# Kernel tuning notes

Measured on AMD Instinct MI355X. Metric: run time of the kernel, lower is better.

## Reference

```python
import jax, jax.numpy as jnp
import numpy as np

D_MODEL = 1024
NUM_HEADS = 16
D_K = D_MODEL // NUM_HEADS
B, S = 4, 2048


def setup_inputs() -> dict:
    key = jax.random.key(0)
    ks = jax.random.split(key, 9)
    scale = 1.0 / np.sqrt(D_MODEL)
    x = jax.random.normal(ks[0], (B, S, D_MODEL), dtype=jnp.float32)
    Wq = jax.random.uniform(ks[1], (D_MODEL, D_MODEL), jnp.float32, -scale, scale)
    bq = jax.random.uniform(ks[2], (D_MODEL,), jnp.float32, -scale, scale)
    Wk = jax.random.uniform(ks[3], (D_MODEL, D_MODEL), jnp.float32, -scale, scale)
    bk = jax.random.uniform(ks[4], (D_MODEL,), jnp.float32, -scale, scale)
    Wv = jax.random.uniform(ks[5], (D_MODEL, D_MODEL), jnp.float32, -scale, scale)
    bv = jax.random.uniform(ks[6], (D_MODEL,), jnp.float32, -scale, scale)
    Wo = jax.random.uniform(ks[7], (D_MODEL, D_MODEL), jnp.float32, -scale, scale)
    bo = jax.random.uniform(ks[8], (D_MODEL,), jnp.float32, -scale, scale)
    return {"x": x, "Wq": Wq, "bq": bq, "Wk": Wk, "bk": bk,
            "Wv": Wv, "bv": bv, "Wo": Wo, "bo": bo}


def reference(x, Wq, bq, Wk, bk, Wv, bv, Wo, bo):
    Bsz, Sl, _ = x.shape
    # Linear: x @ W.T + b (torch nn.Linear convention), then split heads -> (B,H,S,d_k)
    def proj(W, b):
        h = jnp.einsum('bsd,ed->bse', x, W) + b
        return h.reshape(Bsz, Sl, NUM_HEADS, D_K).transpose(0, 2, 1, 3)
    q = proj(Wq, bq)
    k = proj(Wk, bk)
    v = proj(Wv, bv)
    scores = jnp.einsum('bhqd,bhkd->bhqk', q, k) / np.sqrt(D_K)
    causal = jnp.tril(jnp.ones((Sl, Sl), dtype=bool))  # True = keep
    scores = jnp.where(causal[None, None], scores, -jnp.inf)
    attn = jax.nn.softmax(scores, axis=-1)
    out = jnp.einsum('bhqk,bhkd->bhqd', attn, v)
    out = out.transpose(0, 2, 1, 3).reshape(Bsz, Sl, D_MODEL)
    return jnp.einsum('bsd,ed->bse', out, Wo) + bo
```

## Files before the change

### kernel.cpp

```cpp
#include <hip/hip_runtime.h>
#include <hip/hip_bf16.h>

typedef __attribute__((ext_vector_type(8))) short short8;
typedef __attribute__((ext_vector_type(4))) short short4v;
typedef __attribute__((ext_vector_type(4))) float floatx4;
typedef __attribute__((ext_vector_type(2))) unsigned int uint2v;
typedef unsigned short u16;

#define B_SZ 4
#define NH   16
#define SEQ  2048
#define DM   1024
#define DK   64
#define M_ROWS (B_SZ * SEQ)

__device__ __forceinline__ u16 f2bf(float f) {
  unsigned u = __float_as_uint(f);
  u += 0x7fff + ((u >> 16) & 1);
  return (u16)(u >> 16);
}

__device__ __forceinline__ unsigned cvt_pk_bf16(float lo, float hi) {
  unsigned r;
  asm("v_cvt_pk_bf16_f32 %0, %1, %2" : "=v"(r) : "v"(lo), "v"(hi));
  return r;
}

__device__ __forceinline__ void async_copy16(const u16* g, const short* lds) {
  __builtin_amdgcn_global_load_lds(
      (const __attribute__((address_space(1))) void*)g,
      (__attribute__((address_space(3))) void*)lds,
      16, 0, 0);
}

#define BAR() do { __builtin_amdgcn_s_barrier(); asm volatile("" ::: "memory"); } while (0)

__global__ __launch_bounds__(256)
void cvt4_kernel(const float* __restrict__ x,
                 const float* __restrict__ wq, const float* __restrict__ wk,
                 const float* __restrict__ wv,
                 u16* __restrict__ xb, u16* __restrict__ wb)
{
  const int y = blockIdx.y;
  const float* src; u16* dst; int n4;
  if (y == 0)      { src = x;  dst = xb;                 n4 = (M_ROWS * DM) / 4; }
  else if (y == 1) { src = wq; dst = wb;                 n4 = (DM * DM) / 4; }
  else if (y == 2) { src = wk; dst = wb + DM * DM;       n4 = (DM * DM) / 4; }
  else             { src = wv; dst = wb + 2 * DM * DM;   n4 = (DM * DM) / 4; }
  for (int i = blockIdx.x * 256 + threadIdx.x; i < n4; i += gridDim.x * 256) {
    floatx4 v = ((const floatx4*)src)[i];
    short4v s;
#pragma unroll
    for (int e = 0; e < 4; ++e) s[e] = (short)f2bf(v[e]);
    ((short4v*)dst)[i] = s;
  }
}

__global__ __launch_bounds__(256)
void cvt1_kernel(const float* __restrict__ in, u16* __restrict__ out, int n4)
{
  for (int i = blockIdx.x * 256 + threadIdx.x; i < n4; i += gridDim.x * 256) {
    floatx4 v = ((const floatx4*)in)[i];
    short4v s;
#pragma unroll
    for (int e = 0; e < 4; ++e) s[e] = (short)f2bf(v[e]);
    ((short4v*)out)[i] = s;
  }
}

__device__ __forceinline__ void stage_half32(
    const u16* __restrict__ src,
    short* dst,
    int wid, int lane)
{
  const int row = wid * 16 + (lane >> 2);
  const int cu  = (lane & 3) ^ ((lane >> 2) & 3) ^ ((lane >> 4) & 3);
  async_copy16(src + (size_t)row * DM + cu * 8, dst + wid * 512);
}

template<int MIF>
__device__ __forceinline__ void gemm256_core(
    const u16* __restrict__ A, const u16* __restrict__ B,
    int m0, int n0, floatx4 (&acc)[MIF][4])
{
  constexpr int ASH = MIF * 32 * 32;
  constexpr int AH  = MIF / 4;
  constexpr int L   = AH + 2;

  __shared__ short smem[2 * (ASH + 8192)];

  const int tid  = threadIdx.x;
  const int wid  = tid >> 6;
  const int lane = tid & 63;
  const int wm   = wid >> 2, wn = wid & 3;
  const int quad = lane >> 4, l16 = lane & 15;
  const int rswz = (l16 & 3) ^ ((l16 >> 2) & 3);

  short* sA_[2] = { smem,       smem + ASH + 8192 };
  short* sB_[2] = { smem + ASH, smem + 2 * ASH + 8192 };

#pragma unroll
  for (int mi = 0; mi < MIF; ++mi)
#pragma unroll
    for (int ni = 0; ni < 4; ++ni)
      acc[mi][ni] = floatx4{0.f, 0.f, 0.f, 0.f};

  const u16* Abase = A + (size_t)m0 * DM;
  const u16* Bbase = B + (size_t)n0 * DM;

#define STAGE_TILE(kof, c) do {                                              \
    _Pragma("unroll")                                                        \
    for (int u = 0; u < AH; ++u)                                             \
      stage_half32(Abase + (size_t)(u * 128) * DM + (kof),                   \
                   sA_[c] + u * 4096, wid, lane);                            \
    stage_half32(Bbase + (kof),                    sB_[c],        wid, lane); \
    stage_half32(Bbase + (size_t)128 * DM + (kof), sB_[c] + 4096, wid, lane); \
  } while (0)

#define VMCNT_L() do {                                                       \
    if constexpr (L == 4) asm volatile("s_waitcnt vmcnt(4)" ::: "memory");   \
    else                  asm volatile("s_waitcnt vmcnt(3)" ::: "memory");   \
  } while (0)

  STAGE_TILE(0, 0);
  STAGE_TILE(32, 1);
  VMCNT_L();
  BAR();

  short8 af[MIF], bf[4];

  for (int i = 0; i < 16; ++i) {
    const bool nl = (i < 15);
#pragma unroll
    for (int half = 0; half < 2; ++half) {
      short* cA = sA_[half];
      short* cB = sB_[half];
      const int kof_n = (2 * i + 2 + half) * 32;

#pragma unroll
      for (int nt = 0; nt < 2; ++nt)
        bf[nt] = *(const short8*)(cB + (wn * 64 + nt * 16 + l16) * 32
                                     + (((quad) ^ rswz) << 3));
#pragma unroll
      for (int mi = 0; mi < MIF / 2; ++mi)
        af[mi] = *(const short8*)(cA + (wm * (MIF * 16) + mi * 16 + l16) * 32
                                     + (((quad) ^ rswz) << 3));
#pragma unroll
      for (int nt = 2; nt < 4; ++nt)
        bf[nt] = *(const short8*)(cB + (wn * 64 + nt * 16 + l16) * 32
                                     + (((quad) ^ rswz) << 3));
#pragma unroll
      for (int mi = MIF / 2; mi < MIF; ++mi)
        af[mi] = *(const short8*)(cA + (wm * (MIF * 16) + mi * 16 + l16) * 32
                                     + (((quad) ^ rswz) << 3));

      __builtin_amdgcn_s_setprio(1);
#pragma unroll
      for (int mi = 0; mi < MIF / 2; ++mi)
#pragma unroll
        for (int nt = 0; nt < 2; ++nt)
          acc[mi][nt] = __builtin_amdgcn_mfma_f32_16x16x32_bf16(
              af[mi], bf[nt], acc[mi][nt], 0, 0, 0);
#pragma unroll
      for (int mi = 0; mi < MIF / 2; ++mi)
#pragma unroll
        for (int nt = 2; nt < 4; ++nt)
          acc[mi][nt] = __builtin_amdgcn_mfma_f32_16x16x32_bf16(
              af[mi], bf[nt], acc[mi][nt], 0, 0, 0);
#pragma unroll
      for (int mi = MIF / 2; mi < MIF; ++mi)
#pragma unroll
        for (int nt = 2; nt < 4; ++nt)
          acc[mi][nt] = __builtin_amdgcn_mfma_f32_16x16x32_bf16(
              af[mi], bf[nt], acc[mi][nt], 0, 0, 0);
      __builtin_amdgcn_s_setprio(0);

      BAR();

      if (nl) {
        STAGE_TILE(kof_n, half);
        VMCNT_L();
      } else {
        asm volatile("s_waitcnt vmcnt(0)" ::: "memory");
      }

      __builtin_amdgcn_s_setprio(1);
#pragma unroll
      for (int mi = MIF / 2; mi < MIF; ++mi)
#pragma unroll
        for (int nt = 0; nt < 2; ++nt)
          acc[mi][nt] = __builtin_amdgcn_mfma_f32_16x16x32_bf16(
              af[mi], bf[nt], acc[mi][nt], 0, 0, 0);
      __builtin_amdgcn_s_setprio(0);

      BAR();
    }
  }
#undef STAGE_TILE
#undef VMCNT_L
}

__global__ __launch_bounds__(512, 2)
void qkv256_kernel(const u16* __restrict__ xb, const u16* __restrict__ wb,
                   const float* __restrict__ bq, const float* __restrict__ bk,
                   const float* __restrict__ bv,
                   u16* __restrict__ Qo, u16* __restrict__ Ko, u16* __restrict__ Vto)
{
  const int bx = blockIdx.x;
  const int wg = (bx & 7) * 48 + (bx >> 3);
  const int mat = wg >> 7;
  const int r   = wg & 127;

  int m0, n0;
  const u16 *A, *Bm;
  if (mat < 2) { m0 = (r >> 2) * 256; n0 = (r & 3) * 256; A = xb; Bm = wb + (size_t)mat * DM * DM; }
  else         { m0 = (r & 3) * 256;  n0 = (r >> 2) * 256; A = wb + (size_t)2 * DM * DM; Bm = xb; }

  floatx4 acc[8][4];
  gemm256_core<8>(A, Bm, m0, n0, acc);

  const int tid = threadIdx.x;
  const int wid = tid >> 6, lane = tid & 63;
  const int wm = wid >> 2, wn = wid & 3;
  const int quad = lane >> 4, l16 = lane & 15;

  if (mat < 2) {
    u16* dst = (mat == 0) ? Qo : Ko;
    const float* bias = (mat == 0) ? bq : bk;
#pragma unroll
    for (int ni = 0; ni < 4; ++ni) {
      const int n = n0 + wn * 64 + ni * 16 + l16;
      const float bb = bias[n];
      const int h = n >> 6, d = n & 63;
#pragma unroll
      for (int mi = 0; mi < 8; ++mi)
#pragma unroll
        for (int rr = 0; rr < 4; ++rr) {
          const int m = m0 + wm * 128 + mi * 16 + quad * 4 + rr;
          const int b = m >> 11, s = m & 2047;
          dst[((size_t)(b * NH + h) * SEQ + s) * DK + d] = f2bf(acc[mi][ni][rr] + bb);
        }
    }
  } else {
#pragma unroll
    for (int mi = 0; mi < 8; ++mi)
#pragma unroll
      for (int rr = 0; rr < 4; ++rr) {
        const int m = m0 + wm * 128 + mi * 16 + quad * 4 + rr;
        const float bb = bv[m];
        const int h = m >> 6, d = m & 63;
#pragma unroll
        for (int ni = 0; ni < 4; ++ni) {
          const int n = n0 + wn * 64 + ni * 16 + l16;
          const int b = n >> 11, s = n & 2047;
          Vto[((size_t)(b * NH + h) * DK + d) * SEQ + s] = f2bf(acc[mi][ni][rr] + bb);
        }
      }
  }
}

#define AT_STR 72
__global__ __launch_bounds__(256, 2)
void attn_kernel(const u16* __restrict__ Q, const u16* __restrict__ Kx,
                 const u16* __restrict__ Vt, u16* __restrict__ O)
{
  __shared__ short Ks[64 * 64];
  __shared__ short Vs[64 * 64];
  __shared__ __align__(16) short Ps[4 * 16 * AT_STR];

  const int bh  = blockIdx.x;
  const int qtb = 15 - (int)blockIdx.y;
  const int q0  = qtb * 128;
  const int tid = threadIdx.x;
  const int w = tid >> 6, lane = tid & 63;
  const int quad = lane >> 4, l16 = lane & 15;
  const int r8 = lane >> 3, c8 = lane & 7;

  const u16* Qh = Q  + (size_t)bh * SEQ * DK;
  const u16* Kh = Kx + (size_t)bh * SEQ * DK;
  const u16* Vh = Vt + (size_t)bh * DK * SEQ;

  short8 qf[2][2];
#pragma unroll
  for (int qp = 0; qp < 2; ++qp) {
    const int qrow = q0 + w * 32 + qp * 16 + l16;
#pragma unroll
    for (int h = 0; h < 2; ++h)
      qf[qp][h] = *(const short8*)(Qh + (size_t)qrow * DK + h * 32 + quad * 8);
  }

  short8 vone;
#pragma unroll
  for (int j = 0; j < 8; ++j) vone[j] = (l16 == 0) ? (short)0x3F80 : (short)0;

  floatx4 o[2][4], ls[2];
#pragma unroll
  for (int qp = 0; qp < 2; ++qp) {
    ls[qp] = floatx4{0.f, 0.f, 0.f, 0.f};
#pragma unroll
    for (int dt = 0; dt < 4; ++dt) o[qp][dt] = floatx4{0.f, 0.f, 0.f, 0.f};
  }

  const float SC2 = 0.18033688011f;
  const int ktmax = 2 * qtb + 2;
  short* Pw = Ps + w * 16 * AT_STR;

  for (int kt = 0; kt < ktmax; ++kt) {
    const int k0 = kt * 64;
    __syncthreads();
#pragma unroll
    for (int c = 0; c < 2; ++c) {
      const int row8 = w * 16 + c * 8;
      const int sw   = (c8 ^ r8) * 8;
      async_copy16(Kh + (size_t)(k0 + row8 + r8) * DK + sw, Ks + row8 * 64);
      async_copy16(Vh + (size_t)(row8 + r8) * SEQ + k0 + sw, Vs + row8 * 64);
    }
    __syncthreads();

    short8 kf[4][2], vf[4][2];
#pragma unroll
    for (int nt = 0; nt < 4; ++nt)
#pragma unroll
      for (int h = 0; h < 2; ++h) {
        kf[nt][h] = *(const short8*)(Ks + (nt * 16 + l16) * 64 + (((h * 4 + quad) ^ (l16 & 7)) * 8));
        vf[nt][h] = *(const short8*)(Vs + (nt * 16 + l16) * 64 + (((h * 4 + quad) ^ (l16 & 7)) * 8));
      }

#pragma unroll
    for (int qp = 0; qp < 2; ++qp) {
      const int frag0 = q0 + w * 32 + qp * 16;
      if (k0 <= frag0 + 15) {
        floatx4 sc[4];
#pragma unroll
        for (int nt = 0; nt < 4; ++nt) {
          floatx4 z = floatx4{0.f, 0.f, 0.f, 0.f};
          z = __builtin_amdgcn_mfma_f32_16x16x32_bf16(kf[nt][0], qf[qp][0], z, 0, 0, 0);
          z = __builtin_amdgcn_mfma_f32_16x16x32_bf16(kf[nt][1], qf[qp][1], z, 0, 0, 0);
          sc[nt] = z;
        }
        const bool diag = (k0 + 63 > frag0);
        const int qrow = frag0 + l16;
#pragma unroll
        for (int nt = 0; nt < 4; ++nt)
#pragma unroll
          for (int r = 0; r < 4; ++r) {
            float s = sc[nt][r] * SC2;
            if (diag) {
              const int col = k0 + nt * 16 + quad * 4 + r;
              if (col > qrow) s = -1e30f;
            }
            sc[nt][r] = __builtin_amdgcn_exp2f(s);
          }
#pragma unroll
        for (int nt = 0; nt < 4; ++nt) {
          uint2v wv2;
          wv2[0] = cvt_pk_bf16(sc[nt][0], sc[nt][1]);
          wv2[1] = cvt_pk_bf16(sc[nt][2], sc[nt][3]);
          *(short4v*)(Pw + l16 * AT_STR + nt * 16 + quad * 4) =
              __builtin_bit_cast(short4v, wv2);
        }
        asm volatile("" ::: "memory");
        short8 pf[2];
#pragma unroll
        for (int h = 0; h < 2; ++h)
          pf[h] = *(const short8*)(Pw + l16 * AT_STR + h * 32 + quad * 8);
#pragma unroll
        for (int dt = 0; dt < 4; ++dt) {
          o[qp][dt] = __builtin_amdgcn_mfma_f32_16x16x32_bf16(pf[0], vf[dt][0], o[qp][dt], 0, 0, 0);
          o[qp][dt] = __builtin_amdgcn_mfma_f32_16x16x32_bf16(pf[1], vf[dt][1], o[qp][dt], 0, 0, 0);
        }
        ls[qp] = __builtin_amdgcn_mfma_f32_16x16x32_bf16(pf[0], vone, ls[qp], 0, 0, 0);
        ls[qp] = __builtin_amdgcn_mfma_f32_16x16x32_bf16(pf[1], vone, ls[qp], 0, 0, 0);
      }
    }
  }

  const int b = bh >> 4, h = bh & 15;
#pragma unroll
  for (int qp = 0; qp < 2; ++qp) {
    const int frag0 = q0 + w * 32 + qp * 16;
#pragma unroll
    for (int r = 0; r < 4; ++r) {
      const float lv  = __shfl(ls[qp][r], lane & 48);
      const float inv = 1.0f / fmaxf(lv, 1e-20f);
      const int row   = frag0 + quad * 4 + r;
      const size_t base = ((size_t)b * SEQ + row) * DM + h * DK;
#pragma unroll
      for (int dt = 0; dt < 4; ++dt)
        O[base + dt * 16 + l16] = f2bf(o[qp][dt][r] * inv);
    }
  }
}

__global__ __launch_bounds__(512, 2)
void oproj256_kernel(const u16* __restrict__ A, const u16* __restrict__ Wob,
                     const float* __restrict__ bo, float* __restrict__ out)
{
  const int bx = blockIdx.x;
  const int wg = (bx & 7) * 32 + (bx >> 3);
  const int m0 = (wg >> 2) * 128, n0 = (wg & 3) * 256;

  floatx4 acc[4][4];
  gemm256_core<4>(A, Wob, m0, n0, acc);

  const int tid = threadIdx.x;
  const int wid = tid >> 6, lane = tid & 63;
  const int wm = wid >> 2, wn = wid & 3;
  const int quad = lane >> 4, l16 = lane & 15;

#pragma unroll
  for (int ni = 0; ni < 4; ++ni) {
    const int n = n0 + wn * 64 + ni * 16 + l16;
    const float bb = bo[n];
#pragma unroll
    for (int mi = 0; mi < 4; ++mi)
#pragma unroll
      for (int rr = 0; rr < 4; ++rr) {
        const int m = m0 + wm * 64 + mi * 16 + quad * 4 + rr;
        out[(size_t)m * DM + n] = acc[mi][ni][rr] + bb;
      }
  }
}

extern "C" void kernel_launch(void* const* d_in, const int* in_sizes, int n_in,
                              void* d_out, int out_size, void* d_ws, size_t ws_size,
                              hipStream_t stream)
{
  const float* x  = (const float*)d_in[0];
  const float* Wq = (const float*)d_in[1];
  const float* bq = (const float*)d_in[2];
  const float* Wk = (const float*)d_in[3];
  const float* bk = (const float*)d_in[4];
  const float* Wv = (const float*)d_in[5];
  const float* bv = (const float*)d_in[6];
  const float* Wo = (const float*)d_in[7];
  const float* bo = (const float*)d_in[8];
  float* out = (float*)d_out;

  u16* qws  = (u16*)d_ws;
  u16* kws  = qws  + (size_t)M_ROWS * DM;
  u16* vtws = kws  + (size_t)M_ROWS * DM;
  u16* ows  = vtws + (size_t)M_ROWS * DM;

  u16* xb = (u16*)d_out;
  u16* wb = xb + (size_t)M_ROWS * DM;
  u16* wo_b = qws;

  cvt4_kernel  <<<dim3(1024, 4), 256, 0, stream>>>(x, Wq, Wk, Wv, xb, wb);
  qkv256_kernel<<<dim3(384), 512, 0, stream>>>(xb, wb, bq, bk, bv, qws, kws, vtws);
  attn_kernel  <<<dim3(64, 16), 256, 0, stream>>>(qws, kws, vtws, ows);
  cvt1_kernel  <<<dim3(1024), 256, 0, stream>>>(Wo, wo_b, (DM * DM) / 4);
  oproj256_kernel<<<dim3(256), 512, 0, stream>>>(ows, wo_b, bo, out);
}
```

Before: 259.9 us.

## Shrink QKV and output-projection GEMM tiles to 128x128 with 4-wave blocks

Replaces the 256-wide, 8-wave GEMM core with a 128x128 tile core using 4 waves, each computing 64x64. The QKV and output projections now launch four and two times as many blocks, respectively. The aim is better occupancy and finer load balance across CUs, with more blocks resident per CU. The trade is lower data reuse per tile, so more global and L2 traffic for the same FLOPs.

Measured after the change: 250.7 us. 3.5% less time.

```diff
diff --git a/kernel.cpp b/kernel.cpp
--- a/kernel.cpp
+++ b/kernel.cpp
@@ -68,39 +68,44 @@
   }
 }
 
-__device__ __forceinline__ void stage_half32(
-    const u16* __restrict__ src,
-    short* dst,
-    int wid, int lane)
-{
-  const int row = wid * 16 + (lane >> 2);
+__device__ __forceinline__ void stage_tile128(
+    const u16* __restrict__ Asrc, const u16* __restrict__ Bsrc,
+    short* sA, short* sB, int w, int lane)
+{
   const int cu  = (lane & 3) ^ ((lane >> 2) & 3) ^ ((lane >> 4) & 3);
-  async_copy16(src + (size_t)row * DM + cu * 8, dst + wid * 512);
-}
-
-template<int MIF>
-__device__ __forceinline__ void gemm256_core(
+  const int rlo = lane >> 2;
+#pragma unroll
+  for (int j = 0; j < 2; ++j) {
+    const int oct = w * 2 + j;
+    const int row = oct * 16 + rlo;
+    async_copy16(Asrc + (size_t)row * DM + cu * 8, sA + oct * 512);
+  }
+#pragma unroll
+  for (int j = 0; j < 2; ++j) {
+    const int oct = w * 2 + j;
+    const int row = oct * 16 + rlo;
+    async_copy16(Bsrc + (size_t)row * DM + cu * 8, sB + oct * 512);
+  }
+}
+
+__device__ __forceinline__ void gemm128_core(
     const u16* __restrict__ A, const u16* __restrict__ B,
-    int m0, int n0, floatx4 (&acc)[MIF][4])
-{
-  constexpr int ASH = MIF * 32 * 32;
-  constexpr int AH  = MIF / 4;
-  constexpr int L   = AH + 2;
-
-  __shared__ short smem[2 * (ASH + 8192)];
+    int m0, int n0, floatx4 (&acc)[4][4])
+{
+  __shared__ short smem[16384];
 
   const int tid  = threadIdx.x;
-  const int wid  = tid >> 6;
+  const int w    = tid >> 6;
   const int lane = tid & 63;
-  const int wm   = wid >> 2, wn = wid & 3;
+  const int wm   = w >> 1, wn = w & 1;
   const int quad = lane >> 4, l16 = lane & 15;
   const int rswz = (l16 & 3) ^ ((l16 >> 2) & 3);
 
-  short* sA_[2] = { smem,       smem + ASH + 8192 };
-  short* sB_[2] = { smem + ASH, smem + 2 * ASH + 8192 };
-
-#pragma unroll
-  for (int mi = 0; mi < MIF; ++mi)
+  short* sA_[2] = { smem,        smem + 8192 };
+  short* sB_[2] = { smem + 4096, smem + 12288 };
+
+#pragma unroll
+  for (int mi = 0; mi < 4; ++mi)
 #pragma unroll
     for (int ni = 0; ni < 4; ++ni)
       acc[mi][ni] = floatx4{0.f, 0.f, 0.f, 0.f};
@@ -108,26 +113,12 @@
   const u16* Abase = A + (size_t)m0 * DM;
   const u16* Bbase = B + (size_t)n0 * DM;
 
-#define STAGE_TILE(kof, c) do {                                              \
-    _Pragma("unroll")                                                        \
-    for (int u = 0; u < AH; ++u)                                             \
-      stage_half32(Abase + (size_t)(u * 128) * DM + (kof),                   \
-                   sA_[c] + u * 4096, wid, lane);                            \
-    stage_half32(Bbase + (kof),                    sB_[c],        wid, lane); \
-    stage_half32(Bbase + (size_t)128 * DM + (kof), sB_[c] + 4096, wid, lane); \
-  } while (0)
-
-#define VMCNT_L() do {                                                       \
-    if constexpr (L == 4) asm volatile("s_waitcnt vmcnt(4)" ::: "memory");   \
-    else                  asm volatile("s_waitcnt vmcnt(3)" ::: "memory");   \
-  } while (0)
-
-  STAGE_TILE(0, 0);
-  STAGE_TILE(32, 1);
-  VMCNT_L();
+  stage_tile128(Abase,      Bbase,      sA_[0], sB_[0], w, lane);
+  stage_tile128(Abase + 32, Bbase + 32, sA_[1], sB_[1], w, lane);
+  asm volatile("s_waitcnt vmcnt(4)" ::: "memory");
   BAR();
 
-  short8 af[MIF], bf[4];
+  short8 af[4], bf[4];
 
   for (int i = 0; i < 16; ++i) {
     const bool nl = (i < 15);
@@ -140,35 +131,25 @@
 #pragma unroll
       for (int nt = 0; nt < 2; ++nt)
         bf[nt] = *(const short8*)(cB + (wn * 64 + nt * 16 + l16) * 32
-                                     + (((quad) ^ rswz) << 3));
-#pragma unroll
-      for (int mi = 0; mi < MIF / 2; ++mi)
-        af[mi] = *(const short8*)(cA + (wm * (MIF * 16) + mi * 16 + l16) * 32
-                                     + (((quad) ^ rswz) << 3));
+                                     + ((quad ^ rswz) << 3));
+#pragma unroll
+      for (int mi = 0; mi < 4; ++mi)
+        af[mi] = *(const short8*)(cA + (wm * 64 + mi * 16 + l16) * 32
+                                     + ((quad ^ rswz) << 3));
 #pragma unroll
       for (int nt = 2; nt < 4; ++nt)
         bf[nt] = *(const short8*)(cB + (wn * 64 + nt * 16 + l16) * 32
-                                     + (((quad) ^ rswz) << 3));
-#pragma unroll
-      for (int mi = MIF / 2; mi < MIF; ++mi)
-        af[mi] = *(const short8*)(cA + (wm * (MIF * 16) + mi * 16 + l16) * 32
-                                     + (((quad) ^ rswz) << 3));
+                                     + ((quad ^ rswz) << 3));
 
       __builtin_amdgcn_s_setprio(1);
 #pragma unroll
-      for (int mi = 0; mi < MIF / 2; ++mi)
-#pragma unroll
-        for (int nt = 0; nt < 2; ++nt)
+      for (int mi = 0; mi < 2; ++mi)
+#pragma unroll
+        for (int nt = 0; nt < 4; ++nt)
           acc[mi][nt] = __builtin_amdgcn_mfma_f32_16x16x32_bf16(
               af[mi], bf[nt], acc[mi][nt], 0, 0, 0);
 #pragma unroll
-      for (int mi = 0; mi < MIF / 2; ++mi)
-#pragma unroll
-        for (int nt = 2; nt < 4; ++nt)
-          acc[mi][nt] = __builtin_amdgcn_mfma_f32_16x16x32_bf16(
-              af[mi], bf[nt], acc[mi][nt], 0, 0, 0);
-#pragma unroll
-      for (int mi = MIF / 2; mi < MIF; ++mi)
+      for (int mi = 2; mi < 4; ++mi)
 #pragma unroll
         for (int nt = 2; nt < 4; ++nt)
           acc[mi][nt] = __builtin_amdgcn_mfma_f32_16x16x32_bf16(
@@ -178,15 +159,15 @@
       BAR();
 
       if (nl) {
-        STAGE_TILE(kof_n, half);
-        VMCNT_L();
+        stage_tile128(Abase + kof_n, Bbase + kof_n, cA, cB, w, lane);
+        asm volatile("s_waitcnt vmcnt(4)" ::: "memory");
       } else {
         asm volatile("s_waitcnt vmcnt(0)" ::: "memory");
       }
 
       __builtin_amdgcn_s_setprio(1);
 #pragma unroll
-      for (int mi = MIF / 2; mi < MIF; ++mi)
+      for (int mi = 2; mi < 4; ++mi)
 #pragma unroll
         for (int nt = 0; nt < 2; ++nt)
           acc[mi][nt] = __builtin_amdgcn_mfma_f32_16x16x32_bf16(
@@ -196,32 +177,30 @@
       BAR();
     }
   }
-#undef STAGE_TILE
-#undef VMCNT_L
-}
-
-__global__ __launch_bounds__(512, 2)
-void qkv256_kernel(const u16* __restrict__ xb, const u16* __restrict__ wb,
+}
+
+__global__ __launch_bounds__(256, 4)
+void qkv128_kernel(const u16* __restrict__ xb, const u16* __restrict__ wb,
                    const float* __restrict__ bq, const float* __restrict__ bk,
                    const float* __restrict__ bv,
                    u16* __restrict__ Qo, u16* __restrict__ Ko, u16* __restrict__ Vto)
 {
   const int bx = blockIdx.x;
-  const int wg = (bx & 7) * 48 + (bx >> 3);
-  const int mat = wg >> 7;
-  const int r   = wg & 127;
+  const int wg = (bx & 7) * 192 + (bx >> 3);
+  const int mat = wg >> 9;
+  const int r   = wg & 511;
 
   int m0, n0;
   const u16 *A, *Bm;
-  if (mat < 2) { m0 = (r >> 2) * 256; n0 = (r & 3) * 256; A = xb; Bm = wb + (size_t)mat * DM * DM; }
-  else         { m0 = (r & 3) * 256;  n0 = (r >> 2) * 256; A = wb + (size_t)2 * DM * DM; Bm = xb; }
-
-  floatx4 acc[8][4];
-  gemm256_core<8>(A, Bm, m0, n0, acc);
+  if (mat < 2) { m0 = (r >> 3) * 128; n0 = (r & 7) * 128; A = xb; Bm = wb + (size_t)mat * DM * DM; }
+  else         { m0 = (r & 7) * 128;  n0 = (r >> 3) * 128; A = wb + (size_t)2 * DM * DM; Bm = xb; }
+
+  floatx4 acc[4][4];
+  gemm128_core(A, Bm, m0, n0, acc);
 
   const int tid = threadIdx.x;
-  const int wid = tid >> 6, lane = tid & 63;
-  const int wm = wid >> 2, wn = wid & 3;
+  const int w = tid >> 6, lane = tid & 63;
+  const int wm = w >> 1, wn = w & 1;
   const int quad = lane >> 4, l16 = lane & 15;
 
   if (mat < 2) {
@@ -233,20 +212,20 @@
       const float bb = bias[n];
       const int h = n >> 6, d = n & 63;
 #pragma unroll
-      for (int mi = 0; mi < 8; ++mi)
+      for (int mi = 0; mi < 4; ++mi)
 #pragma unroll
         for (int rr = 0; rr < 4; ++rr) {
-          const int m = m0 + wm * 128 + mi * 16 + quad * 4 + rr;
+          const int m = m0 + wm * 64 + mi * 16 + quad * 4 + rr;
           const int b = m >> 11, s = m & 2047;
           dst[((size_t)(b * NH + h) * SEQ + s) * DK + d] = f2bf(acc[mi][ni][rr] + bb);
         }
     }
   } else {
 #pragma unroll
-    for (int mi = 0; mi < 8; ++mi)
+    for (int mi = 0; mi < 4; ++mi)
 #pragma unroll
       for (int rr = 0; rr < 4; ++rr) {
-        const int m = m0 + wm * 128 + mi * 16 + quad * 4 + rr;
+        const int m = m0 + wm * 64 + mi * 16 + quad * 4 + rr;
         const float bb = bv[m];
         const int h = m >> 6, d = m & 63;
 #pragma unroll
@@ -392,20 +371,20 @@
   }
 }
 
-__global__ __launch_bounds__(512, 2)
-void oproj256_kernel(const u16* __restrict__ A, const u16* __restrict__ Wob,
+__global__ __launch_bounds__(256, 4)
+void oproj128_kernel(const u16* __restrict__ A, const u16* __restrict__ Wob,
                      const float* __restrict__ bo, float* __restrict__ out)
 {
   const int bx = blockIdx.x;
-  const int wg = (bx & 7) * 32 + (bx >> 3);
-  const int m0 = (wg >> 2) * 128, n0 = (wg & 3) * 256;
+  const int wg = (bx & 7) * 64 + (bx >> 3);
+  const int m0 = (wg >> 3) * 128, n0 = (wg & 7) * 128;
 
   floatx4 acc[4][4];
-  gemm256_core<4>(A, Wob, m0, n0, acc);
+  gemm128_core(A, Wob, m0, n0, acc);
 
   const int tid = threadIdx.x;
-  const int wid = tid >> 6, lane = tid & 63;
-  const int wm = wid >> 2, wn = wid & 3;
+  const int w = tid >> 6, lane = tid & 63;
+  const int wm = w >> 1, wn = w & 1;
   const int quad = lane >> 4, l16 = lane & 15;
 
 #pragma unroll
@@ -447,8 +426,8 @@
   u16* wo_b = qws;
 
   cvt4_kernel  <<<dim3(1024, 4), 256, 0, stream>>>(x, Wq, Wk, Wv, xb, wb);
-  qkv256_kernel<<<dim3(384), 512, 0, stream>>>(xb, wb, bq, bk, bv, qws, kws, vtws);
+  qkv128_kernel<<<dim3(1536), 256, 0, stream>>>(xb, wb, bq, bk, bv, qws, kws, vtws);
   attn_kernel  <<<dim3(64, 16), 256, 0, stream>>>(qws, kws, vtws, ows);
   cvt1_kernel  <<<dim3(1024), 256, 0, stream>>>(Wo, wo_b, (DM * DM) / 4);
-  oproj256_kernel<<<dim3(256), 512, 0, stream>>>(ows, wo_b, bo, out);
-}
+  oproj128_kernel<<<dim3(512), 256, 0, stream>>>(ows, wo_b, bo, out);
+}
```
